# Performance work log

Measured on AMD Instinct MI355X. Metric: run time of the kernel, lower is better.

## Reference

```python
import jax, jax.numpy as jnp
import numpy as np

N = 1048576  # n_envs (patients)

# param column order in the (N,30) params array
_P = ['BW','KMAX','B','D','KMIN','KABS','F','KP1','KP2','KP3','FSNC','KE1','KE2',
     'K1','K2','VM0','VMX','KM0','M1','M2','M4','KA1','KA2','VI','P2U','IB','KI',
     'M30','KD','KSC']
_IDX = {n: i for i, n in enumerate(_P)}


def setup_inputs() -> dict:
    key = jax.random.key(0)
    ks = jax.random.split(key, 6)
    # positive, well-conditioned values (B < 1, divisors bounded away from 0)
    x = jax.random.uniform(ks[0], (N, 13), jnp.float32, 0.1, 2.0)
    params = jax.random.uniform(ks[1], (N, 30), jnp.float32, 0.5, 0.95)
    action_ins = jax.random.uniform(ks[2], (N, 1), jnp.float32, 0.0, 1.0)
    action_CHO = jax.random.uniform(ks[3], (N, 1), jnp.float32, 0.0, 1.0)
    last_Qsto = jax.random.uniform(ks[4], (N, 1), jnp.float32, 0.0, 1.0)
    last_foodtaken = jax.random.uniform(ks[5], (N, 1), jnp.float32, 0.0, 1.0)
    return {'x': x, 'params': params, 'action_ins': action_ins,
            'action_CHO': action_CHO, 'last_Qsto': last_Qsto,
            'last_foodtaken': last_foodtaken}


def _dxdt(x, params, action_ins, action_CHO, last_Qsto, last_foodtaken):
    p = lambda n: params[:, _IDX[n]:_IDX[n] + 1]  # (N,1) column
    xs = [x[:, i:i + 1] for i in range(13)]

    BW = p('BW'); KMAX = p('KMAX'); B = p('B'); D = p('D'); KMIN = p('KMIN')
    KABS = p('KABS'); F = p('F'); KP1 = p('KP1'); KP2 = p('KP2'); KP3 = p('KP3')
    FSNC = p('FSNC'); KE1 = p('KE1'); KE2 = p('KE2'); K1 = p('K1'); K2 = p('K2')
    VM0 = p('VM0'); VMX = p('VMX'); KM0 = p('KM0'); M1 = p('M1'); M2 = p('M2')
    M4 = p('M4'); KA1 = p('KA1'); KA2 = p('KA2'); VI = p('VI'); P2U = p('P2U')
    IB = p('IB'); KI = p('KI'); M30 = p('M30'); KD = p('KD'); KSC = p('KSC')

    f_insulin = action_ins * 6000.0 / BW
    qsto = xs[0] + xs[1]
    Dbar = last_Qsto + last_foodtaken

    dx0 = -KMAX * xs[0] + action_CHO * 1000.0

    aa = 5.0 / 2.0 / (1.0 - B) / (Dbar + 1e-7)
    cc = 5.0 / 2.0 / D / (Dbar + 1e-7)
    kgut_true = KMIN + (KMAX - KMIN) / 2.0 * (
        jnp.tanh(aa * (qsto - B * Dbar)) - jnp.tanh(cc * (qsto - D * Dbar)) + 2.0)
    kgut = jnp.where(Dbar > 0, kgut_true, KMAX)

    dx1 = KMAX * xs[0] - xs[1] * kgut
    dx2 = kgut * xs[1] - KABS * xs[2]

    Rat = F * KABS * xs[2] / BW
    EGPt = KP1 - KP2 * xs[3] - KP3 * xs[8]
    Et = jnp.where(xs[3] > KE2, KE1 * (xs[3] - KE2), 0.0)
    dx3 = jnp.maximum(EGPt, 0.0) + Rat - FSNC - Et - K1 * xs[3] + K2 * xs[4]
    dx3 = jnp.where(xs[3] >= 0, dx3, 0.0)

    Vmt = VM0 + VMX * xs[6]
    Uidt = Vmt * xs[4] / (KM0 + xs[4])
    dx4 = -Uidt + K1 * xs[3] - K2 * xs[4]
    dx4 = jnp.where(xs[4] >= 0, dx4, 0.0)

    dx5 = -(M2 + M4) * xs[5] + M1 * xs[9] + KA1 * xs[10] + KA2 * xs[11]
    It = xs[5] / VI
    dx5 = jnp.where(xs[5] >= 0, dx5, 0.0)

    dx6 = -P2U * xs[6] + P2U * (It - IB)
    dx7 = -KI * (xs[7] - It)
    dx8 = -KI * (xs[8] - xs[7])

    dx9 = -(M1 + M30) * xs[9] + M2 * xs[5]
    dx9 = jnp.where(xs[9] >= 0, dx9, 0.0)

    dx10 = f_insulin - (KA1 + KD) * xs[10]
    dx10 = jnp.where(xs[10] >= 0, dx10, 0.0)

    dx11 = KD * xs[10] - KA2 * xs[11]
    dx11 = jnp.where(xs[11] >= 0, dx11, 0.0)

    dx12 = -KSC * xs[12] + KSC * xs[3]
    dx12 = jnp.where(xs[12] >= 0, dx12, 0.0)

    return jnp.concatenate(
        [dx0, dx1, dx2, dx3, dx4, dx5, dx6, dx7, dx8, dx9, dx10, dx11, dx12],
        axis=1)  # (N, 13)


def reference(x, params, action_ins, action_CHO, last_Qsto, last_foodtaken):
    return _dxdt(x, params, action_ins, action_CHO, last_Qsto, last_foodtaken)
```

## Files before the change

kernel.cpp:

```cpp
#include <hip/hip_runtime.h>
#include <math.h>

#define WAVE 64
#define XW 13
#define PW 30
#define NBLOCK 3584

typedef float f4 __attribute__((ext_vector_type(4)));

__device__ __forceinline__ void dxdt(const float* X, const float* P,
                                     float ai, float cho, float lq, float lf,
                                     float* dx)
{
    const float BW = P[0],  KMAX = P[1],  B   = P[2],  D   = P[3],  KMIN = P[4];
    const float KABS = P[5], F   = P[6],  KP1 = P[7],  KP2 = P[8],  KP3  = P[9];
    const float FSNC = P[10], KE1 = P[11], KE2 = P[12], K1 = P[13], K2   = P[14];
    const float VM0 = P[15], VMX = P[16], KM0 = P[17], M1 = P[18], M2   = P[19];
    const float M4  = P[20], KA1 = P[21], KA2 = P[22], VI = P[23], P2U  = P[24];
    const float IB  = P[25], KI  = P[26], M30 = P[27], KD = P[28], KSC  = P[29];

    const float f_insulin = ai * 6000.0f / BW;
    const float qsto = X[0] + X[1];
    const float Dbar = lq + lf;

    dx[0] = -KMAX * X[0] + cho * 1000.0f;

    const float inv_dbar = 1.0f / (Dbar + 1e-7f);
    const float aa = 2.5f / (1.0f - B) * inv_dbar;
    const float cc = 2.5f / D * inv_dbar;
    const float kgut_true = KMIN + (KMAX - KMIN) * 0.5f *
        (tanhf(aa * (qsto - B * Dbar)) - tanhf(cc * (qsto - D * Dbar)) + 2.0f);
    const float kgut = (Dbar > 0.0f) ? kgut_true : KMAX;

    dx[1] = KMAX * X[0] - X[1] * kgut;
    dx[2] = kgut * X[1] - KABS * X[2];

    const float Rat  = F * KABS * X[2] / BW;
    const float EGPt = KP1 - KP2 * X[3] - KP3 * X[8];
    const float Et   = (X[3] > KE2) ? KE1 * (X[3] - KE2) : 0.0f;
    const float d3 = fmaxf(EGPt, 0.0f) + Rat - FSNC - Et - K1 * X[3] + K2 * X[4];
    dx[3] = (X[3] >= 0.0f) ? d3 : 0.0f;

    const float Vmt  = VM0 + VMX * X[6];
    const float Uidt = Vmt * X[4] / (KM0 + X[4]);
    const float d4 = -Uidt + K1 * X[3] - K2 * X[4];
    dx[4] = (X[4] >= 0.0f) ? d4 : 0.0f;

    const float d5 = -(M2 + M4) * X[5] + M1 * X[9] + KA1 * X[10] + KA2 * X[11];
    const float It = X[5] / VI;
    dx[5] = (X[5] >= 0.0f) ? d5 : 0.0f;

    dx[6] = -P2U * X[6] + P2U * (It - IB);
    dx[7] = -KI * (X[7] - It);
    dx[8] = -KI * (X[8] - X[7]);

    const float d9 = -(M1 + M30) * X[9] + M2 * X[5];
    dx[9] = (X[9] >= 0.0f) ? d9 : 0.0f;

    const float d10 = f_insulin - (KA1 + KD) * X[10];
    dx[10] = (X[10] >= 0.0f) ? d10 : 0.0f;

    const float d11 = KD * X[10] - KA2 * X[11];
    dx[11] = (X[11] >= 0.0f) ? d11 : 0.0f;

    const float d12 = -KSC * X[12] + KSC * X[3];
    dx[12] = (X[12] >= 0.0f) ? d12 : 0.0f;
}

__global__ __launch_bounds__(WAVE, 2) void t1d_kernel(
    const float* __restrict__ x,
    const float* __restrict__ params,
    const float* __restrict__ action_ins,
    const float* __restrict__ action_CHO,
    const float* __restrict__ last_Qsto,
    const float* __restrict__ last_foodtaken,
    float* __restrict__ out, int n)
{
    __shared__ __align__(16) float xb[WAVE * XW];
    __shared__ __align__(16) float pb[WAVE * PW];

    const int l = threadIdx.x;
    const int ntiles = n / WAVE;
    f4* xl4 = (f4*)xb;
    f4* pl4 = (f4*)pb;

    int t = (int)blockIdx.x;
    if (t < ntiles) {
        size_t base = (size_t)t * WAVE;
        const f4* xg = (const f4*)(x + base * XW);
        const f4* pg = (const f4*)(params + base * PW);
        f4 a0 = __builtin_nontemporal_load(xg + l);
        f4 a1 = __builtin_nontemporal_load(xg + l + 64);
        f4 a2 = __builtin_nontemporal_load(xg + l + 128);
        f4 a3;
        if (l < 16) a3 = __builtin_nontemporal_load(xg + 192 + l);
        f4 b0 = __builtin_nontemporal_load(pg + l);
        f4 b1 = __builtin_nontemporal_load(pg + l + 64);
        f4 b2 = __builtin_nontemporal_load(pg + l + 128);
        f4 b3 = __builtin_nontemporal_load(pg + l + 192);
        f4 b4 = __builtin_nontemporal_load(pg + l + 256);
        f4 b5 = __builtin_nontemporal_load(pg + l + 320);
        f4 b6 = __builtin_nontemporal_load(pg + l + 384);
        f4 b7;
        if (l < 32) b7 = __builtin_nontemporal_load(pg + 448 + l);
        float ai  = __builtin_nontemporal_load(action_ins + base + l);
        float cho = __builtin_nontemporal_load(action_CHO + base + l);
        float lq  = __builtin_nontemporal_load(last_Qsto + base + l);
        float lf  = __builtin_nontemporal_load(last_foodtaken + base + l);

        #pragma clang loop unroll(disable)
        for (;;) {
            xl4[l]       = a0;
            xl4[l + 64]  = a1;
            xl4[l + 128] = a2;
            if (l < 16) xl4[192 + l] = a3;
            pl4[l]       = b0;
            pl4[l + 64]  = b1;
            pl4[l + 128] = b2;
            pl4[l + 192] = b3;
            pl4[l + 256] = b4;
            pl4[l + 320] = b5;
            pl4[l + 384] = b6;
            if (l < 32) pl4[448 + l] = b7;

            const float  cai = ai, ccho = cho, clq = lq, clf = lf;
            const size_t obase = (size_t)t * WAVE;

            const int  tn   = t + (int)gridDim.x;
            const bool more = tn < ntiles;
            if (more) {
                size_t nb = (size_t)tn * WAVE;
                const f4* xg2 = (const f4*)(x + nb * XW);
                const f4* pg2 = (const f4*)(params + nb * PW);
                a0 = __builtin_nontemporal_load(xg2 + l);
                a1 = __builtin_nontemporal_load(xg2 + l + 64);
                a2 = __builtin_nontemporal_load(xg2 + l + 128);
                if (l < 16) a3 = __builtin_nontemporal_load(xg2 + 192 + l);
                b0 = __builtin_nontemporal_load(pg2 + l);
                b1 = __builtin_nontemporal_load(pg2 + l + 64);
                b2 = __builtin_nontemporal_load(pg2 + l + 128);
                b3 = __builtin_nontemporal_load(pg2 + l + 192);
                b4 = __builtin_nontemporal_load(pg2 + l + 256);
                b5 = __builtin_nontemporal_load(pg2 + l + 320);
                b6 = __builtin_nontemporal_load(pg2 + l + 384);
                if (l < 32) b7 = __builtin_nontemporal_load(pg2 + 448 + l);
                ai  = __builtin_nontemporal_load(action_ins + nb + l);
                cho = __builtin_nontemporal_load(action_CHO + nb + l);
                lq  = __builtin_nontemporal_load(last_Qsto + nb + l);
                lf  = __builtin_nontemporal_load(last_foodtaken + nb + l);
            }

            float X[XW], P[PW], dx[XW];
            #pragma unroll
            for (int j = 0; j < XW; ++j) X[j] = xb[l * XW + j];
            #pragma unroll
            for (int j = 0; j < PW; ++j) P[j] = pb[l * PW + j];

            dxdt(X, P, cai, ccho, clq, clf, dx);

            #pragma unroll
            for (int j = 0; j < XW; ++j) xb[l * XW + j] = dx[j];
            f4 o0 = xl4[l], o1 = xl4[l + 64], o2 = xl4[l + 128], o3;
            if (l < 16) o3 = xl4[192 + l];
            f4* og = (f4*)(out + obase * XW);
            __builtin_nontemporal_store(o0, og + l);
            __builtin_nontemporal_store(o1, og + l + 64);
            __builtin_nontemporal_store(o2, og + l + 128);
            if (l < 16) __builtin_nontemporal_store(o3, og + 192 + l);

            if (!more) break;
            t = tn;
        }
    }

    const int tail0 = ntiles * WAVE;
    for (int i = tail0 + (int)blockIdx.x * WAVE + l; i < n;
         i += (int)gridDim.x * WAVE) {
        float X[XW], P[PW], dx[XW];
        #pragma unroll
        for (int j = 0; j < XW; ++j) X[j] = x[(size_t)i * XW + j];
        #pragma unroll
        for (int j = 0; j < PW; ++j) P[j] = params[(size_t)i * PW + j];
        dxdt(X, P, action_ins[i], action_CHO[i], last_Qsto[i],
             last_foodtaken[i], dx);
        #pragma unroll
        for (int j = 0; j < XW; ++j) out[(size_t)i * XW + j] = dx[j];
    }
}

extern "C" void kernel_launch(void* const* d_in, const int* in_sizes, int n_in,
                              void* d_out, int out_size, void* d_ws, size_t ws_size,
                              hipStream_t stream) {
    const float* x      = (const float*)d_in[0];
    const float* params = (const float*)d_in[1];
    const float* ai     = (const float*)d_in[2];
    const float* cho    = (const float*)d_in[3];
    const float* lq     = (const float*)d_in[4];
    const float* lf     = (const float*)d_in[5];
    float* out = (float*)d_out;

    const int n = in_sizes[0] / XW;
    const int ntiles = n / WAVE;
    int grid = ntiles > 0 ? (ntiles < NBLOCK ? ntiles : NBLOCK) : 1;
    t1d_kernel<<<grid, WAVE, 0, stream>>>(x, params, ai, cho, lq, lf, out, n);
}
```

Baseline: 234.4 us.

## Replace persistent grid-stride loop with one-tile-per-block launch

Drops the persistent 3584-block grid that software-prefetched the next tile into registers while computing the current one. Instead it launches one 64-thread block per tile (16384 blocks) and relies on hardware block scheduling and occupancy to hide memory latency. Partial tiles are handled in an else branch with per-element global loads. This removes loop overhead and prefetch register pressure, but gives up the explicit load/compute overlap and adds block launch overhead.

```diff
diff --git a/kernel.cpp b/kernel.cpp
--- a/kernel.cpp
+++ b/kernel.cpp
@@ -4,7 +4,6 @@
 #define WAVE 64
 #define XW 13
 #define PW 30
-#define NBLOCK 3584
 
 typedef float f4 __attribute__((ext_vector_type(4)));
 
@@ -80,15 +79,14 @@
     __shared__ __align__(16) float pb[WAVE * PW];
 
     const int l = threadIdx.x;
-    const int ntiles = n / WAVE;
+    const size_t base = (size_t)blockIdx.x * WAVE;
     f4* xl4 = (f4*)xb;
     f4* pl4 = (f4*)pb;
 
-    int t = (int)blockIdx.x;
-    if (t < ntiles) {
-        size_t base = (size_t)t * WAVE;
+    if (base + WAVE <= (size_t)n) {
         const f4* xg = (const f4*)(x + base * XW);
         const f4* pg = (const f4*)(params + base * PW);
+
         f4 a0 = __builtin_nontemporal_load(xg + l);
         f4 a1 = __builtin_nontemporal_load(xg + l + 64);
         f4 a2 = __builtin_nontemporal_load(xg + l + 128);
@@ -103,88 +101,54 @@
         f4 b6 = __builtin_nontemporal_load(pg + l + 384);
         f4 b7;
         if (l < 32) b7 = __builtin_nontemporal_load(pg + 448 + l);
-        float ai  = __builtin_nontemporal_load(action_ins + base + l);
-        float cho = __builtin_nontemporal_load(action_CHO + base + l);
-        float lq  = __builtin_nontemporal_load(last_Qsto + base + l);
-        float lf  = __builtin_nontemporal_load(last_foodtaken + base + l);
+        const float ai  = __builtin_nontemporal_load(action_ins + base + l);
+        const float cho = __builtin_nontemporal_load(action_CHO + base + l);
+        const float lq  = __builtin_nontemporal_load(last_Qsto + base + l);
+        const float lf  = __builtin_nontemporal_load(last_foodtaken + base + l);
 
-        #pragma clang loop unroll(disable)
-        for (;;) {
-            xl4[l]       = a0;
-            xl4[l + 64]  = a1;
-            xl4[l + 128] = a2;
-            if (l < 16) xl4[192 + l] = a3;
-            pl4[l]       = b0;
-            pl4[l + 64]  = b1;
-            pl4[l + 128] = b2;
-            pl4[l + 192] = b3;
-            pl4[l + 256] = b4;
-            pl4[l + 320] = b5;
-            pl4[l + 384] = b6;
-            if (l < 32) pl4[448 + l] = b7;
+        xl4[l]       = a0;
+        xl4[l + 64]  = a1;
+        xl4[l + 128] = a2;
+        if (l < 16) xl4[192 + l] = a3;
+        pl4[l]       = b0;
+        pl4[l + 64]  = b1;
+        pl4[l + 128] = b2;
+        pl4[l + 192] = b3;
+        pl4[l + 256] = b4;
+        pl4[l + 320] = b5;
+        pl4[l + 384] = b6;
+        if (l < 32) pl4[448 + l] = b7;
 
-            const float  cai = ai, ccho = cho, clq = lq, clf = lf;
-            const size_t obase = (size_t)t * WAVE;
+        float X[XW], P[PW], dx[XW];
+        #pragma unroll
+        for (int j = 0; j < XW; ++j) X[j] = xb[l * XW + j];
+        #pragma unroll
+        for (int j = 0; j < PW; ++j) P[j] = pb[l * PW + j];
 
-            const int  tn   = t + (int)gridDim.x;
-            const bool more = tn < ntiles;
-            if (more) {
-                size_t nb = (size_t)tn * WAVE;
-                const f4* xg2 = (const f4*)(x + nb * XW);
-                const f4* pg2 = (const f4*)(params + nb * PW);
-                a0 = __builtin_nontemporal_load(xg2 + l);
-                a1 = __builtin_nontemporal_load(xg2 + l + 64);
-                a2 = __builtin_nontemporal_load(xg2 + l + 128);
-                if (l < 16) a3 = __builtin_nontemporal_load(xg2 + 192 + l);
-                b0 = __builtin_nontemporal_load(pg2 + l);
-                b1 = __builtin_nontemporal_load(pg2 + l + 64);
-                b2 = __builtin_nontemporal_load(pg2 + l + 128);
-                b3 = __builtin_nontemporal_load(pg2 + l + 192);
-                b4 = __builtin_nontemporal_load(pg2 + l + 256);
-                b5 = __builtin_nontemporal_load(pg2 + l + 320);
-                b6 = __builtin_nontemporal_load(pg2 + l + 384);
-                if (l < 32) b7 = __builtin_nontemporal_load(pg2 + 448 + l);
-                ai  = __builtin_nontemporal_load(action_ins + nb + l);
-                cho = __builtin_nontemporal_load(action_CHO + nb + l);
-                lq  = __builtin_nontemporal_load(last_Qsto + nb + l);
-                lf  = __builtin_nontemporal_load(last_foodtaken + nb + l);
-            }
+        dxdt(X, P, ai, cho, lq, lf, dx);
 
+        #pragma unroll
+        for (int j = 0; j < XW; ++j) xb[l * XW + j] = dx[j];
+        f4 o0 = xl4[l], o1 = xl4[l + 64], o2 = xl4[l + 128], o3;
+        if (l < 16) o3 = xl4[192 + l];
+        f4* og = (f4*)(out + base * XW);
+        __builtin_nontemporal_store(o0, og + l);
+        __builtin_nontemporal_store(o1, og + l + 64);
+        __builtin_nontemporal_store(o2, og + l + 128);
+        if (l < 16) __builtin_nontemporal_store(o3, og + 192 + l);
+    } else {
+        const size_t i = base + l;
+        if (i < (size_t)n) {
             float X[XW], P[PW], dx[XW];
             #pragma unroll
-            for (int j = 0; j < XW; ++j) X[j] = xb[l * XW + j];
+            for (int j = 0; j < XW; ++j) X[j] = x[i * XW + j];
             #pragma unroll
-            for (int j = 0; j < PW; ++j) P[j] = pb[l * PW + j];
-
-            dxdt(X, P, cai, ccho, clq, clf, dx);
-
+            for (int j = 0; j < PW; ++j) P[j] = params[i * PW + j];
+            dxdt(X, P, action_ins[i], action_CHO[i], last_Qsto[i],
+                 last_foodtaken[i], dx);
             #pragma unroll
-            for (int j = 0; j < XW; ++j) xb[l * XW + j] = dx[j];
-            f4 o0 = xl4[l], o1 = xl4[l + 64], o2 = xl4[l + 128], o3;
-            if (l < 16) o3 = xl4[192 + l];
-            f4* og = (f4*)(out + obase * XW);
-            __builtin_nontemporal_store(o0, og + l);
-            __builtin_nontemporal_store(o1, og + l + 64);
-            __builtin_nontemporal_store(o2, og + l + 128);
-            if (l < 16) __builtin_nontemporal_store(o3, og + 192 + l);
-
-            if (!more) break;
-            t = tn;
+            for (int j = 0; j < XW; ++j) out[i * XW + j] = dx[j];
         }
-    }
-
-    const int tail0 = ntiles * WAVE;
-    for (int i = tail0 + (int)blockIdx.x * WAVE + l; i < n;
-         i += (int)gridDim.x * WAVE) {
-        float X[XW], P[PW], dx[XW];
-        #pragma unroll
-        for (int j = 0; j < XW; ++j) X[j] = x[(size_t)i * XW + j];
-        #pragma unroll
-        for (int j = 0; j < PW; ++j) P[j] = params[(size_t)i * PW + j];
-        dxdt(X, P, action_ins[i], action_CHO[i], last_Qsto[i],
-             last_foodtaken[i], dx);
-        #pragma unroll
-        for (int j = 0; j < XW; ++j) out[(size_t)i * XW + j] = dx[j];
     }
 }
 
@@ -200,7 +164,6 @@
     float* out = (float*)d_out;
 
     const int n = in_sizes[0] / XW;
-    const int ntiles = n / WAVE;
-    int grid = ntiles > 0 ? (ntiles < NBLOCK ? ntiles : NBLOCK) : 1;
+    const int grid = (n + WAVE - 1) / WAVE;
     t1d_kernel<<<grid, WAVE, 0, stream>>>(x, params, ai, cho, lq, lf, out, n);
 }
```

Measured after the change: 229.2 us. -2.2%, faster.
